# Performance work log

Hardware: AMD Instinct MI355X
Metric: run time of the kernel (lower is better)

The kernel has to match this reference:

```python
import jax, jax.numpy as jnp
import numpy as np

K = 8
EPS = 1e-5

def knn_idx(x, k):
    # x: (B, C, N) -> idx (B, N, k) nearest neighbors (incl. self)
    xt = jnp.swapaxes(x, 1, 2)  # (B, N, C)
    inner = -2.0 * jnp.einsum('bnc,bmc->bnm', xt, xt)
    xx = jnp.sum(xt * xt, axis=-1)  # (B, N)
    neg_dist = -xx[:, :, None] - inner - xx[:, None, :]
    return jax.lax.top_k(neg_dist, k)[1]

def graph_feature(x, k):
    # x: (B, C, N) -> (B, 2C, N, k)
    B, C, N = x.shape
    idx = knn_idx(x, k)  # (B, N, k)
    xt = jnp.swapaxes(x, 1, 2)  # (B, N, C)
    nb = xt[jnp.arange(B)[:, None, None], idx]  # (B, N, k, C)
    center = xt[:, :, None, :]
    feat = jnp.concatenate([nb - center, jnp.broadcast_to(center, nb.shape)], axis=-1)
    return jnp.transpose(feat, (0, 3, 1, 2))

def bn2d(h, g, b):
    m = jnp.mean(h, axis=(0, 2, 3), keepdims=True)
    v = jnp.var(h, axis=(0, 2, 3), keepdims=True)
    return g[None, :, None, None] * (h - m) * jax.lax.rsqrt(v + EPS) + b[None, :, None, None]

def bn1d(h, g, b):
    m = jnp.mean(h, axis=(0, 2), keepdims=True)
    v = jnp.var(h, axis=(0, 2), keepdims=True)
    return g[None, :, None] * (h - m) * jax.lax.rsqrt(v + EPS) + b[None, :, None]

def fps_idx(xyz, m):
    # xyz: (B, N, 3) furthest point sampling starting at index 0 -> (B, m) int32
    B, N, _ = xyz.shape
    def body(carry, _):
        dist, last = carry
        lastp = jnp.take_along_axis(xyz, last[:, None, None], axis=1)  # (B,1,3)
        d = jnp.sum((xyz - lastp) ** 2, axis=-1)
        dist = jnp.minimum(dist, d)
        nxt = jnp.argmax(dist, axis=-1).astype(jnp.int32)
        return (dist, nxt), last
    init = (jnp.full((B, N), 1e10, dtype=xyz.dtype), jnp.zeros((B,), jnp.int32))
    _, idxs = jax.lax.scan(body, init, None, length=m)
    return jnp.swapaxes(idxs, 0, 1)  # (B, m)

def fps_downsample(coor, x, m):
    # coor: (B,3,N), x: (B,C,N)
    idx = fps_idx(jnp.swapaxes(coor, 1, 2), m)  # (B, m)
    B = coor.shape[0]
    comb = jnp.concatenate([coor, x], axis=1)  # (B, 3+C, N)
    g = jnp.take_along_axis(comb, idx[:, None, :], axis=2)
    return g[:, :3], g[:, 3:]

def edge_block(h, w, g, b):
    f = graph_feature(h, K)                      # (B, 2C, N, k)
    f = jnp.einsum('oc,bcnk->bonk', w, f)        # 1x1 conv2d, no bias
    f = jax.nn.leaky_relu(bn2d(f, g, b), 0.2)
    return jnp.max(f, axis=-1)                   # (B, O, N)

def setup_inputs() -> dict:
    key = jax.random.key(0)
    ks = jax.random.split(key, 16)
    H = 2048
    c16, c8, c4, c2 = H // 16, H // 8, H // 4, H // 2  # 128,256,512,1024
    O2 = 4096 // 2  # 2048
    def w(k, o, c):
        return jax.random.normal(k, (o, c), jnp.float32) * (1.0 / np.sqrt(c))
    inp = {
        'x': jax.random.normal(ks[0], (8, 3, 2048), jnp.float32),
        'w1': w(ks[1], c16, 6),
        'w2': w(ks[2], c16, c8),
        'w3': w(ks[3], c8, c8),
        'w4': w(ks[4], c4, c4),
        'w5': w(ks[5], O2, c2),
        'rw1': w(ks[6], c16, c16),
        'rw2': w(ks[7], c8, c16),
        'rw3': w(ks[8], c4, c8),
    }
    for i, (nm, ch) in enumerate([('1', c16), ('2', c16), ('3', c8), ('4', c4), ('5', O2)]):
        kk = jax.random.split(ks[9 + i], 2)
        inp['g' + nm] = 1.0 + 0.1 * jax.random.normal(kk[0], (ch,), jnp.float32)
        inp['b' + nm] = 0.1 * jax.random.normal(kk[1], (ch,), jnp.float32)
    return inp

def reference(x, w1, w2, w3, w4, w5, rw1, rw2, rw3, g1, b1, g2, b2, g3, b3, g4, b4, g5, b5):
    coor = x
    x1 = edge_block(x, w1, g1, b1)
    x2 = edge_block(x1, w2, g2, b2) + jnp.einsum('oc,bcn->bon', rw1, x1)
    x3 = edge_block(x2, w3, g3, b3) + jnp.einsum('oc,bcn->bon', rw2, x2)
    x4 = edge_block(x3, w4, g4, b4) + jnp.einsum('oc,bcn->bon', rw3, x3)
    h = jnp.concatenate([x1, x2, x3, x4], axis=1)  # (B, 1024, N)
    h = jax.nn.leaky_relu(bn1d(jnp.einsum('oc,bcn->bon', w5, h), g5, b5), 0.2)
    for m in (512, 256, 128):
        coor, h = fps_downsample(coor, h, m)
    f = jnp.concatenate([jnp.max(h, axis=-1), jnp.mean(h, axis=-1)], axis=1)  # (B, 4096)
    return coor, f
```

## Files before the change

### kernel.cpp

```cpp
#include <hip/hip_runtime.h>
#include <float.h>

#define NPTS 2048
#define NB 8
#define KNN 8

__device__ __forceinline__ float leakyf(float x){ return x > 0.f ? x : 0.2f*x; }

#define BET(v1,i1,v2,i2) (((v1)>(v2)) || ((v1)==(v2) && (i1)<(i2)))

__device__ __forceinline__ void ins8(float tv[8], int tix[8], float v, int ci)
{
    if (BET(v,ci,tv[7],tix[7])){
        tv[7]=v; tix[7]=ci;
#pragma unroll
        for (int q=7;q>=1;q--){
            if (BET(tv[q],tix[q],tv[q-1],tix[q-1])){
                float t=tv[q]; tv[q]=tv[q-1]; tv[q-1]=t;
                int ti=tix[q]; tix[q]=tix[q-1]; tix[q-1]=ti;
            }
        }
    }
}

__device__ __forceinline__ void merge_write8(float tv[8], int tix[8], int lane,
                                             int* __restrict__ dst)
{
#pragma unroll
    for (int r=0;r<8;r++){
        float bv = tv[0]; int bi = tix[0];
#pragma unroll
        for (int off=32; off; off>>=1){
            float ov = __shfl_xor(bv, off); int oi = __shfl_xor(bi, off);
            if (BET(ov,oi,bv,bi)){ bv=ov; bi=oi; }
        }
        if (tv[0]==bv && tix[0]==bi){
#pragma unroll
            for (int q=0;q<7;q++){ tv[q]=tv[q+1]; tix[q]=tix[q+1]; }
            tv[7]=-FLT_MAX; tix[7]=0x7fffffff;
        }
        if (lane==0) dst[r] = bi;
    }
}

__global__ void transpose_x(const float* __restrict__ x, float* __restrict__ xt)
{
    int g = blockIdx.x*256 + threadIdx.x;
    if (g >= NB*NPTS) return;
    int b = g >> 11, n = g & 2047;
    const float* xb = x + (long)b*3*NPTS;
    xt[g*3+0] = xb[n];
    xt[g*3+1] = xb[NPTS+n];
    xt[g*3+2] = xb[2*NPTS+n];
}

__device__ __forceinline__ unsigned long long u64max(unsigned long long a,
                                                     unsigned long long b)
{ return a > b ? a : b; }

template<int CTRL>
__device__ __forceinline__ unsigned long long dpp_max_step(unsigned long long v)
{
    unsigned plo = (unsigned)__builtin_amdgcn_update_dpp(0, (int)(unsigned)v,      CTRL, 0xF, 0xF, true);
    unsigned phi = (unsigned)__builtin_amdgcn_update_dpp(0, (int)(unsigned)(v>>32), CTRL, 0xF, 0xF, true);
    unsigned long long p = ((unsigned long long)phi << 32) | plo;
    return u64max(v, p);
}

__device__ __forceinline__ unsigned long long wave_reduce_max(unsigned long long v)
{
    v = dpp_max_step<0x111>(v);
    v = dpp_max_step<0x112>(v);
    v = dpp_max_step<0x114>(v);
    v = dpp_max_step<0x118>(v);
    v = dpp_max_step<0x142>(v);
    v = dpp_max_step<0x143>(v);
    return v;
}

template<int NPP>
__device__ void fps_stage_mw(const float4* __restrict__ pts, int m, int* sel,
                             int tid, unsigned long long* wv )
{
    float cx[NPP], cy[NPP], cz[NPP], dist[NPP];
#pragma unroll
    for (int r=0;r<NPP;r++){
        float4 p = pts[r*256 + tid];
        cx[r]=p.x; cy[r]=p.y; cz[r]=p.z; dist[r]=1e10f;
    }
    int w = tid>>6, lane = tid&63;
    int last = 0;
    if (tid==0) sel[0]=0;
    for (int i=1;i<m;i++){
        float4 lp = pts[last];
#pragma unroll
        for (int r=0;r<NPP;r++){
            float dx=__fsub_rn(cx[r],lp.x), dy=__fsub_rn(cy[r],lp.y), dz=__fsub_rn(cz[r],lp.z);
            float d = __fadd_rn(__fadd_rn(__fmul_rn(dx,dx), __fmul_rn(dy,dy)), __fmul_rn(dz,dz));
            dist[r] = fminf(dist[r], d);
        }
        unsigned long long t[(NPP+1)/2];
        if (NPP == 1){
            t[0] = ((unsigned long long)__float_as_uint(dist[0])<<32) | (unsigned)(2047 - tid);
        } else {
#pragma unroll
            for (int k=0;k<NPP/2;k++){
                unsigned long long a = ((unsigned long long)__float_as_uint(dist[2*k  ])<<32) | (unsigned)(2047 - ((2*k  )*256+tid));
                unsigned long long b = ((unsigned long long)__float_as_uint(dist[2*k+1])<<32) | (unsigned)(2047 - ((2*k+1)*256+tid));
                t[k] = u64max(a, b);
            }
#pragma unroll
            for (int s=NPP/4; s>=1; s>>=1)
#pragma unroll
                for (int k=0;k<s;k++) t[k] = u64max(t[k], t[k+s]);
        }
        unsigned long long best = wave_reduce_max(t[0]);
        if (lane==63) wv[(i&1)*4 + w] = best;
        __syncthreads();
        unsigned long long b0 = wv[(i&1)*4+0], b1 = wv[(i&1)*4+1];
        unsigned long long b2 = wv[(i&1)*4+2], b3 = wv[(i&1)*4+3];
        best = u64max(u64max(b0,b1), u64max(b2,b3));
        int win = 2047 - (int)(unsigned)best;
        last = win;
        if (tid==0) sel[i] = win;
    }
}

__global__ __launch_bounds__(256)
void knn_c3(const float* __restrict__ x, int* __restrict__ idx)
{
    __shared__ float sx[NPTS], sy[NPTS], sz[NPTS];
    int b = blockIdx.x >> 5, rblk = blockIdx.x & 31;
    const float* xb = x + (long)b*3*NPTS;
    int tid = threadIdx.x;
    for (int i=tid;i<NPTS;i+=256){
        sx[i]=xb[i]; sy[i]=xb[NPTS+i]; sz[i]=xb[2*NPTS+i];
    }
    __syncthreads();
    int w = tid>>6, lane = tid&63;
    for (int rr=0; rr<16; rr++){
        int n = rblk*64 + w*16 + rr;
        float px=sx[n], py=sy[n], pz=sz[n];
        float tv[8]; int tix[8];
#pragma unroll
        for (int i=0;i<8;i++){ tv[i]=-FLT_MAX; tix[i]=0x7fffffff; }
        for (int it=0; it<8; it++){
            int c = it*256 + lane*4;
            float4 qx = *(const float4*)&sx[c];
            float4 qy = *(const float4*)&sy[c];
            float4 qz = *(const float4*)&sz[c];
            float dx, dy, dz;
            dx=qx.x-px; dy=qy.x-py; dz=qz.x-pz;
            ins8(tv,tix, -fmaf(dx,dx,fmaf(dy,dy,dz*dz)), c+0);
            dx=qx.y-px; dy=qy.y-py; dz=qz.y-pz;
            ins8(tv,tix, -fmaf(dx,dx,fmaf(dy,dy,dz*dz)), c+1);
            dx=qx.z-px; dy=qy.z-py; dz=qz.z-pz;
            ins8(tv,tix, -fmaf(dx,dx,fmaf(dy,dy,dz*dz)), c+2);
            dx=qx.w-px; dy=qy.w-py; dz=qz.w-pz;
            ins8(tv,tix, -fmaf(dx,dx,fmaf(dy,dy,dz*dz)), c+3);
        }
        merge_write8(tv, tix, lane, idx + ((long)(b*NPTS+n))*KNN);
    }
}

__global__ void prep_w(const float* __restrict__ w, const float* __restrict__ rw,
                       float* __restrict__ wcat, int O, int C, int hasR)
{
    int t = blockIdx.x*256 + threadIdx.x;
    if (t >= O*C) return;
    int o = t / C, c = t % C;
    float a = w[o*2*C + c];
    wcat[o*C + c] = a;
    wcat[(O+o)*C + c] = w[o*2*C + C + c] - a;
    if (hasR) wcat[(2*O+o)*C + c] = rw[o*C + c];
}

__global__ void rownorm(const float* __restrict__ X, float* __restrict__ xx,
                        int lda, int C)
{
    int g = blockIdx.x*256 + threadIdx.x;
    if (g >= NB*NPTS) return;
    const float* r = X + (long)g*lda;
    float s = 0.f;
    for (int c=0;c<C;c++) s += r[c]*r[c];
    xx[g] = s;
}

template<int VEC, bool SYM>
__global__ __launch_bounds__(256)
void gemm_nt(const float* __restrict__ A, const float* __restrict__ B,
             float* __restrict__ C,
             int M, int Nc, int Kd, int lda, int ldb, int ldc,
             long sA, long sB, long sC)
{
    if (SYM && blockIdx.y > blockIdx.x) return;
    int bz = blockIdx.z;
    A += (long)bz * sA; B += (long)bz * sB; C += (long)bz * sC;
    int tm = blockIdx.y * 128, tn = blockIdx.x * 128;
    __shared__ __align__(16) float As[16][132];
    __shared__ __align__(16) float Bs[16][132];
    int tid = threadIdx.x;
    int ty = tid >> 4, tx = tid & 15;
    int cn0 = tx*4, cn1 = 64 + tx*4;
    float acc[8][8] = {};
    for (int k0 = 0; k0 < Kd; k0 += 16){
        if (VEC == 4){
#pragma unroll
            for (int i=0;i<2;i++){
                int e = tid + i*256;
                int rr = e >> 2, kq = e & 3;
                float4 av = *(const float4*)(A + (long)(tm+rr)*lda + k0 + kq*4);
                float4 bv = *(const float4*)(B + (long)(tn+rr)*ldb + k0 + kq*4);
                As[kq*4+0][rr]=av.x; As[kq*4+1][rr]=av.y; As[kq*4+2][rr]=av.z; As[kq*4+3][rr]=av.w;
                Bs[kq*4+0][rr]=bv.x; Bs[kq*4+1][rr]=bv.y; Bs[kq*4+2][rr]=bv.z; Bs[kq*4+3][rr]=bv.w;
            }
        } else {
#pragma unroll
            for (int i=0;i<8;i++){
                int e = tid + i*256;
                int kk = e & 15, rr = e >> 4;
                int ak = k0 + kk;
                As[kk][rr] = (ak < Kd) ? A[(long)(tm+rr)*lda + ak] : 0.f;
                Bs[kk][rr] = (ak < Kd) ? B[(long)(tn+rr)*ldb + ak] : 0.f;
            }
        }
        __syncthreads();
#pragma unroll
        for (int kk=0;kk<16;kk++){
            float4 a01 = *(const float4*)&As[kk][ty*8];
            float4 a23 = *(const float4*)&As[kk][ty*8+4];
            float4 b01 = *(const float4*)&Bs[kk][cn0];
            float4 b23 = *(const float4*)&Bs[kk][cn1];
            float aa[8] = {a01.x,a01.y,a01.z,a01.w,a23.x,a23.y,a23.z,a23.w};
            float bb[8] = {b01.x,b01.y,b01.z,b01.w,b23.x,b23.y,b23.z,b23.w};
#pragma unroll
            for (int i=0;i<8;i++)
#pragma unroll
                for (int j=0;j<8;j++)
                    acc[i][j] += aa[i]*bb[j];
        }
        __syncthreads();
    }
#pragma unroll
    for (int i=0;i<8;i++){
        long r = tm + ty*8 + i;
        float4 v0 = {acc[i][0],acc[i][1],acc[i][2],acc[i][3]};
        float4 v1 = {acc[i][4],acc[i][5],acc[i][6],acc[i][7]};
        *(float4*)(C + r*ldc + tn + cn0) = v0;
        *(float4*)(C + r*ldc + tn + cn1) = v1;
    }
    if (SYM && blockIdx.x != blockIdx.y){
#pragma unroll
        for (int j=0;j<4;j++){
            long r0 = tn + cn0 + j;
            long r1 = tn + cn1 + j;
            float4 u0 = {acc[0][j],  acc[1][j],  acc[2][j],  acc[3][j]};
            float4 u1 = {acc[4][j],  acc[5][j],  acc[6][j],  acc[7][j]};
            float4 u2 = {acc[0][j+4],acc[1][j+4],acc[2][j+4],acc[3][j+4]};
            float4 u3 = {acc[4][j+4],acc[5][j+4],acc[6][j+4],acc[7][j+4]};
            *(float4*)(C + r0*ldc + tm + ty*8)     = u0;
            *(float4*)(C + r0*ldc + tm + ty*8 + 4) = u1;
            *(float4*)(C + r1*ldc + tm + ty*8)     = u2;
            *(float4*)(C + r1*ldc + tm + ty*8 + 4) = u3;
        }
    }
}

__global__ __launch_bounds__(256)
void topk8(const float* __restrict__ D, const float* __restrict__ xx,
           int* __restrict__ idx, int b0)
{
    int tid = threadIdx.x, w = tid>>6, lane = tid & 63;
    int gr = blockIdx.x*4 + w;
    int b = b0 + (gr >> 11);
    const float* drow = D + (long)gr*NPTS;
    const float* xb = xx + (long)b*NPTS;
    float tv[8]; int tix[8];
#pragma unroll
    for (int i=0;i<8;i++){ tv[i]=-FLT_MAX; tix[i]=0x7fffffff; }
    for (int it=0; it<8; it++){
        int c = it*256 + lane*4;
        float4 d4 = *(const float4*)(drow + c);
        float4 x4 = *(const float4*)(xb + c);
        ins8(tv,tix, 2.f*d4.x - x4.x, c+0);
        ins8(tv,tix, 2.f*d4.y - x4.y, c+1);
        ins8(tv,tix, 2.f*d4.z - x4.z, c+2);
        ins8(tv,tix, 2.f*d4.w - x4.w, c+3);
    }
    merge_write8(tv, tix, lane, idx + ((long)(b0*NPTS) + gr)*KNN);
}

__global__ __launch_bounds__(256)
void stats_edge(const float* __restrict__ uvr, const int* __restrict__ idx,
                float* __restrict__ ps, float* __restrict__ pq,
                float* __restrict__ mxb, float* __restrict__ mnb,
                int O, int ld)
{
    int tid = threadIdx.x;
    int r0 = blockIdx.x * 128;
    float s0=0,q0=0,s1=0,q1=0;
    for (int rr=0; rr<128; rr++){
        int g = r0 + rr;
        int b = g >> 11;
        const int* ip = idx + (long)g*KNN;
        const float* vrow = uvr + (long)g*ld + O;
        const float* ub[8];
#pragma unroll
        for (int k=0;k<8;k++) ub[k] = uvr + (long)((b<<11) + ip[k])*ld;
        int o = tid;
        if (o < O){
            float vv = vrow[o];
            float mx=-FLT_MAX, mn=FLT_MAX;
#pragma unroll
            for (int k=0;k<8;k++){
                float f = ub[k][o]+vv;
                s0+=f; q0+=f*f; mx=fmaxf(mx,f); mn=fminf(mn,f);
            }
            mxb[(long)g*O+o]=mx; mnb[(long)g*O+o]=mn;
        }
        o = tid + 256;
        if (o < O){
            float vv = vrow[o];
            float mx=-FLT_MAX, mn=FLT_MAX;
#pragma unroll
            for (int k=0;k<8;k++){
                float f = ub[k][o]+vv;
                s1+=f; q1+=f*f; mx=fmaxf(mx,f); mn=fminf(mn,f);
            }
            mxb[(long)g*O+o]=mx; mnb[(long)g*O+o]=mn;
        }
    }
    if (tid < O){ ps[blockIdx.x*2048 + tid] = s0; pq[blockIdx.x*2048 + tid] = q0; }
    if (tid+256 < O){ ps[blockIdx.x*2048 + tid+256] = s1; pq[blockIdx.x*2048 + tid+256] = q1; }
}

__global__ void reduce_stats(const float* __restrict__ ps, const float* __restrict__ pq,
                             const float* __restrict__ gam, const float* __restrict__ bet,
                             float* __restrict__ ab, float* __restrict__ cb,
                             int O, int np, float invCnt)
{
    int o = blockIdx.x*256 + threadIdx.x;
    if (o >= O) return;
    float s=0.f, q=0.f;
    for (int p=0;p<np;p++){ s += ps[p*2048 + o]; q += pq[p*2048 + o]; }
    float m = s * invCnt;
    float var = q * invCnt - m*m;
    float a = gam[o] * rsqrtf(var + 1e-5f);
    ab[o] = a;
    cb[o] = bet[o] - m*a;
}

__global__ void finalize_edge(const float* __restrict__ mxb, const float* __restrict__ mnb,
                              const float* __restrict__ uvr,
                              const float* __restrict__ ab, const float* __restrict__ cb,
                              float* __restrict__ hcat, int lgO, int ld, int hoff, int hasR)
{
    long t = (long)blockIdx.x*256 + threadIdx.x;
    int O = 1 << lgO;
    int o = (int)(t & (O-1));
    int g = (int)(t >> lgO);
    float a = ab[o], c = cb[o];
    float mx = mxb[t], mn = mnb[t];
    float zz = (a > 0.f) ? (a*mx + c) : (a*mn + c);
    float outv = leakyf(zz);
    if (hasR) outv += uvr[(long)g*ld + 2*O + o];
    hcat[(long)g*1024 + hoff + o] = outv;
}

__global__ void colsum_part(const float* __restrict__ H, float* __restrict__ part)
{
    int pb = blockIdx.x;
    int tid = threadIdx.x;
    const float4* h4 = (const float4*)(H + (long)pb*128*1024);
    float4 acc = {0,0,0,0};
    for (int r=0;r<128;r++){
        float4 v = h4[r*256 + tid];
        acc.x+=v.x; acc.y+=v.y; acc.z+=v.z; acc.w+=v.w;
    }
    ((float4*)part)[pb*256 + tid] = acc;
}
__global__ void colsum_fin(const float* __restrict__ part, float* __restrict__ hbar)
{
    int tid = threadIdx.x;
    float4 acc = {0,0,0,0};
    for (int p=0;p<128;p++){
        float4 v = ((const float4*)part)[p*256 + tid];
        acc.x+=v.x; acc.y+=v.y; acc.z+=v.z; acc.w+=v.w;
    }
    ((float4*)hbar)[tid] = acc;
}

struct FpsSh {
    float4 pts1[2048]; float4 pts2[512]; float4 pts3[256];
    int sel1[512]; int sel2[256]; int sel3[128];
    unsigned long long wv[8];
};
struct GramSh { __align__(16) float As[32][132]; __align__(16) float Bs[32][132]; };
union ShU { FpsSh f; GramSh g; };

__global__ __launch_bounds__(256)
void gram_fps(const float* __restrict__ A, float* __restrict__ P,
              const float* __restrict__ x, int* __restrict__ idxF,
              float* __restrict__ coorOut)
{
    __shared__ ShU sh;
    int tid = threadIdx.x;
    if (blockIdx.x < 8){
        int b = blockIdx.x;
        const float* xb = x + (long)b*3*NPTS;
        for (int i=tid;i<2048;i+=256)
            sh.f.pts1[i] = make_float4(xb[i], xb[NPTS+i], xb[2*NPTS+i], 0.f);
        __syncthreads();
        fps_stage_mw<8>(sh.f.pts1, 512, sh.f.sel1, tid, sh.f.wv);
        __syncthreads();
        for (int i=tid;i<512;i+=256) sh.f.pts2[i] = sh.f.pts1[sh.f.sel1[i]];
        __syncthreads();
        fps_stage_mw<2>(sh.f.pts2, 256, sh.f.sel2, tid, sh.f.wv);
        __syncthreads();
        for (int i=tid;i<256;i+=256) sh.f.pts3[i] = sh.f.pts2[sh.f.sel2[i]];
        __syncthreads();
        fps_stage_mw<1>(sh.f.pts3, 128, sh.f.sel3, tid, sh.f.wv);
        __syncthreads();
        for (int i=tid;i<128;i+=256){
            int gi = sh.f.sel1[sh.f.sel2[sh.f.sel3[i]]];
            idxF[b*128+i] = gi;
            float4 p = sh.f.pts1[gi];
            coorOut[(long)b*384 + 0*128 + i] = p.x;
            coorOut[(long)b*384 + 1*128 + i] = p.y;
            coorOut[(long)b*384 + 2*128 + i] = p.z;
        }
        return;
    }
    int id8 = blockIdx.x - 8;
    int bx = id8 & 7, by = (id8 >> 3) & 7, bz = id8 >> 6;
    if (by < bx) return;
    int ti = by*128, tj = bx*128;
    int ty = tid>>4, tx = tid&15;
    float acc[8][8] = {};
    const float* Abase = A + (long)bz*1024*1024;
    for (int k0=0; k0<1024; k0+=32){
#pragma unroll
        for (int i=0;i<4;i++){
            int e = tid + i*256;
            int mm = e>>5, c4 = (e&31)*4;
            const float* arow = Abase + (long)(k0+mm)*1024;
            *(float4*)&sh.g.As[mm][c4] = *(const float4*)(arow + ti + c4);
            *(float4*)&sh.g.Bs[mm][c4] = *(const float4*)(arow + tj + c4);
        }
        __syncthreads();
#pragma unroll
        for (int mm=0;mm<32;mm++){
            float4 a01 = *(const float4*)&sh.g.As[mm][ty*8];
            float4 a23 = *(const float4*)&sh.g.As[mm][ty*8+4];
            float4 b01 = *(const float4*)&sh.g.Bs[mm][tx*4];
            float4 b23 = *(const float4*)&sh.g.Bs[mm][64+tx*4];
            float aa[8] = {a01.x,a01.y,a01.z,a01.w,a23.x,a23.y,a23.z,a23.w};
            float bb[8] = {b01.x,b01.y,b01.z,b01.w,b23.x,b23.y,b23.z,b23.w};
#pragma unroll
            for (int i=0;i<8;i++)
#pragma unroll
                for (int j=0;j<8;j++)
                    acc[i][j] += aa[i]*bb[j];
        }
        __syncthreads();
    }
    float* Pp = P + ((long)bz<<20);
#pragma unroll
    for (int i=0;i<8;i++){
        long r = ti + ty*8 + i;
        float4 v0 = {acc[i][0],acc[i][1],acc[i][2],acc[i][3]};
        float4 v1 = {acc[i][4],acc[i][5],acc[i][6],acc[i][7]};
        *(float4*)(Pp + r*1024 + tj + tx*4)      = v0;
        *(float4*)(Pp + r*1024 + tj + 64 + tx*4) = v1;
    }
}

__global__ void greduce(const float* __restrict__ P, float* __restrict__ G)
{
    long i4 = (long)blockIdx.x*256 + threadIdx.x;
    float4 a = ((const float4*)P)[i4];
    for (int p=1;p<16;p++){
        float4 v = ((const float4*)P)[((long)p<<18) + i4];
        a.x+=v.x; a.y+=v.y; a.z+=v.z; a.w+=v.w;
    }
    ((float4*)G)[i4] = a;
}

__global__ void mirror_g(float* __restrict__ G)
{
    __shared__ float t[64][65];
    int q = blockIdx.x, I = 0, acc = 15;
    while (q >= acc){ q -= acc; acc--; I++; }
    int J = I + 1 + q;
    int tid = threadIdx.x;
#pragma unroll
    for (int k=0;k<16;k++){
        int e = tid + k*256;
        int sr = e>>6, sc = e&63;
        t[sr][sc] = G[(long)(J*64+sr)*1024 + I*64+sc];
    }
    __syncthreads();
#pragma unroll
    for (int k=0;k<16;k++){
        int e = tid + k*256;
        int dr = e>>6, dc = e&63;
        G[(long)(I*64+dr)*1024 + J*64+dc] = t[dc][dr];
    }
}

__global__ void bn5_prep(const float* __restrict__ w5, const float* __restrict__ T,
                         const float* __restrict__ hbar,
                         const float* __restrict__ g5, const float* __restrict__ b5,
                         float* __restrict__ ab, float* __restrict__ cb)
{
    int w = threadIdx.x>>6, lane = threadIdx.x&63;
    int n = blockIdx.x*4 + w;
    const float4* wr = (const float4*)(w5 + (long)n*1024);
    const float4* tr = (const float4*)(T  + (long)n*1024);
    const float4* hb = (const float4*)hbar;
    float s1=0.f, s2=0.f;
    for (int i=lane;i<256;i+=64){
        float4 wv = wr[i], t4 = tr[i], hv = hb[i];
        s1 += wv.x*hv.x + wv.y*hv.y + wv.z*hv.z + wv.w*hv.w;
        s2 += wv.x*t4.x + wv.y*t4.y + wv.z*t4.z + wv.w*t4.w;
    }
#pragma unroll
    for (int off=32; off; off>>=1){
        s1 += __shfl_xor(s1, off);
        s2 += __shfl_xor(s2, off);
    }
    if (lane==0){
        float m = s1*(1.f/16384.f);
        float qq = s2*(1.f/16384.f);
        float var = qq - m*m;
        float a = g5[n]*rsqrtf(var+1e-5f);
        ab[n]=a; cb[n]=b5[n]-m*a;
    }
}

__global__ void gather_rows(const float* __restrict__ src, const int* __restrict__ idxF,
                            float* __restrict__ dst)
{
    int r = blockIdx.x;
    int b = r >> 7;
    int srow = (b<<11) + idxF[r];
    const float4* s = (const float4*)(src + (long)srow*1024);
    float4* d = (float4*)(dst + (long)r*1024);
    for (int c=threadIdx.x; c<256; c+=256) d[c] = s[c];
}

__global__ void finalize_f(const float* __restrict__ zsel, const float* __restrict__ ab,
                           const float* __restrict__ cb, float* __restrict__ out)
{
    int b = blockIdx.x >> 3, oc = blockIdx.x & 7;
    int o = oc*256 + threadIdx.x;
    float a = ab[o], c = cb[o];
    float mx = -FLT_MAX, sm = 0.f;
    const float* zp = zsel + (long)b*128*2048 + o;
    for (int i=0;i<128;i++){
        float v = leakyf(a*zp[(long)i*2048] + c);
        mx = fmaxf(mx, v); sm += v;
    }
    out[b*4096 + o] = mx;
    out[b*4096 + 2048 + o] = sm * (1.f/128.f);
}

extern "C" void kernel_launch(void* const* d_in, const int* in_sizes, int n_in,
                              void* d_out, int out_size, void* d_ws, size_t ws_size,
                              hipStream_t stream)
{
    (void)in_sizes; (void)n_in; (void)out_size; (void)ws_size;
    const float* x   = (const float*)d_in[0];
    const float* w1  = (const float*)d_in[1];
    const float* w2  = (const float*)d_in[2];
    const float* w3  = (const float*)d_in[3];
    const float* w4  = (const float*)d_in[4];
    const float* w5  = (const float*)d_in[5];
    const float* rw1 = (const float*)d_in[6];
    const float* rw2 = (const float*)d_in[7];
    const float* rw3 = (const float*)d_in[8];
    const float* g1  = (const float*)d_in[9];  const float* b1 = (const float*)d_in[10];
    const float* g2  = (const float*)d_in[11]; const float* b2 = (const float*)d_in[12];
    const float* g3  = (const float*)d_in[13]; const float* b3 = (const float*)d_in[14];
    const float* g4  = (const float*)d_in[15]; const float* b4 = (const float*)d_in[16];
    const float* g5  = (const float*)d_in[17]; const float* b5 = (const float*)d_in[18];
    float* out = (float*)d_out;

    char* wsb = (char*)d_ws;
    size_t off = 0;
    auto alloc = [&](size_t bytes)->char* {
        char* p = wsb + off;
        off += (bytes + 255) & ~(size_t)255;
        return p;
    };
    float* xt    = (float*)alloc((size_t)16384*3*4);
    float* hcat  = (float*)alloc((size_t)16384*1024*4);
    float* uvr   = (float*)alloc((size_t)16384*1536*4);
    float* Dbuf  = uvr;
    float* gramP = uvr;
    float* G     = (float*)alloc((size_t)1024*1024*4);
    float* T     = (float*)alloc((size_t)2048*1024*4);
    float* zselA = (float*)alloc((size_t)1024*1024*4);
    float* zsel  = (float*)alloc((size_t)1024*2048*4);
    float* mxb   = (float*)alloc((size_t)16384*512*4);
    float* mnb   = (float*)alloc((size_t)16384*512*4);
    float* xx    = (float*)alloc((size_t)16384*4);
    int*   idx   = (int*)  alloc((size_t)16384*8*4);
    float* wcat  = (float*)alloc((size_t)1536*256*4);
    float* ps    = (float*)alloc((size_t)128*2048*4);
    float* pq    = (float*)alloc((size_t)128*2048*4);
    float* cspart= (float*)alloc((size_t)128*1024*4);
    float* hbar  = (float*)alloc((size_t)1024*4);
    float* ab    = (float*)alloc((size_t)2048*4);
    float* cb    = (float*)alloc((size_t)2048*4);
    int*   idxF  = (int*)  alloc((size_t)1024*4);

    transpose_x<<<64, 256, 0, stream>>>(x, xt);

    struct EB {
        const float* X; int lda, C, O, lgO, hoff, hasR;
        const float* w; const float* rw; const float* g; const float* bb;
    };
    EB eb[4] = {
        { xt,        3,    3,   128, 7, 0,   0, w1, nullptr, g1, b1 },
        { hcat+0,    1024, 128, 128, 7, 128, 1, w2, rw1,     g2, b2 },
        { hcat+128,  1024, 128, 256, 8, 256, 1, w3, rw2,     g3, b3 },
        { hcat+256,  1024, 256, 512, 9, 512, 1, w4, rw3,     g4, b4 },
    };
    for (int i=0;i<4;i++){
        EB e = eb[i];
        int ld = (2 + e.hasR) * e.O;
        int tot = e.O * e.C;
        prep_w<<<(tot+255)/256, 256, 0, stream>>>(e.w, e.rw, wcat, e.O, e.C, e.hasR);
        if (i == 0){
            knn_c3<<<256, 256, 0, stream>>>(x, idx);
            gemm_nt<1,false><<<dim3(ld/128, 128, 1), 256, 0, stream>>>(
                e.X, wcat, uvr, 16384, ld, e.C, e.lda, e.C, ld, 0, 0, 0);
        } else {
            rownorm<<<64, 256, 0, stream>>>(e.X, xx, e.lda, e.C);
            for (int b0=0; b0<8; b0+=2){
                const float* Ab = e.X + (long)b0*NPTS*e.lda;
                gemm_nt<4,true><<<dim3(16,16,2), 256, 0, stream>>>(
                    Ab, Ab, Dbuf, 2048, 2048, e.C, e.lda, e.lda, 2048,
                    (long)NPTS*e.lda, (long)NPTS*e.lda, (long)NPTS*NPTS);
                topk8<<<1024, 256, 0, stream>>>(Dbuf, xx, idx, b0);
            }
            gemm_nt<4,false><<<dim3(ld/128, 128, 1), 256, 0, stream>>>(
                e.X, wcat, uvr, 16384, ld, e.C, e.lda, e.C, ld, 0, 0, 0);
        }
        stats_edge<<<128, 256, 0, stream>>>(uvr, idx, ps, pq, mxb, mnb, e.O, ld);
        reduce_stats<<<(e.O+255)/256, 256, 0, stream>>>(ps, pq, e.g, e.bb, ab, cb,
                                                        e.O, 128, 1.f/131072.f);
        finalize_edge<<<64*e.O, 256, 0, stream>>>(mxb, mnb, uvr, ab, cb, hcat,
                                                  e.lgO, ld, e.hoff, e.hasR);
    }

    colsum_part<<<128, 256, 0, stream>>>(hcat, cspart);
    colsum_fin<<<1, 256, 0, stream>>>(cspart, hbar);
    gram_fps<<<8 + 8*8*16, 256, 0, stream>>>(hcat, gramP, x, idxF, out);
    greduce<<<1024, 256, 0, stream>>>(gramP, G);
    mirror_g<<<120, 256, 0, stream>>>(G);
    gemm_nt<4,false><<<dim3(8,16,1), 256, 0, stream>>>(
        w5, G, T, 2048, 1024, 1024, 1024, 1024, 1024, 0, 0, 0);
    bn5_prep<<<512, 256, 0, stream>>>(w5, T, hbar, g5, b5, ab, cb);
    gather_rows<<<1024, 256, 0, stream>>>(hcat, idxF, zselA);
    gemm_nt<4,false><<<dim3(16,8,1), 256, 0, stream>>>(
        zselA, w5, zsel, 1024, 2048, 1024, 1024, 1024, 2048, 0, 0, 0);
    finalize_f<<<64, 256, 0, stream>>>(zsel, ab, cb, out + 3072);
}
```

Before: 3.524 ms.

## Use bf16 MFMA for Gram matrix and move FPS into the last edge GEMM launch

The Gram matrix of the concatenated features is now computed with bf16 MFMA instructions over swizzled LDS tiles, one upper-triangle tile per batch, and the column-sum work is fused into the same launch. FPS runs alongside the layer-4 uvr GEMM blocks instead of alongside the Gram blocks, so it overlaps with different work. kNN for the first layer uses four times as many smaller blocks, and the distance GEMM and top-k batches are processed four at a time instead of two. Rounding the Gram inputs to bf16 lowers the precision of the BN5 statistics, which may move results outside tolerance.

```diff
diff --git a/kernel.cpp b/kernel.cpp
--- a/kernel.cpp
+++ b/kernel.cpp
@@ -5,7 +5,15 @@
 #define NB 8
 #define KNN 8
 
+typedef short bf16x8 __attribute__((ext_vector_type(8)));
+typedef float f32x4  __attribute__((ext_vector_type(4)));
+
 __device__ __forceinline__ float leakyf(float x){ return x > 0.f ? x : 0.2f*x; }
+
+__device__ __forceinline__ unsigned short f2bf(float f){
+    unsigned u = __float_as_uint(f);
+    return (unsigned short)((u + 0x7FFF + ((u>>16)&1)) >> 16);
+}
 
 #define BET(v1,i1,v2,i2) (((v1)>(v2)) || ((v1)==(v2) && (i1)<(i2)))
 
@@ -80,7 +88,7 @@
 
 template<int NPP>
 __device__ void fps_stage_mw(const float4* __restrict__ pts, int m, int* sel,
-                             int tid, unsigned long long* wv )
+                             int tid, unsigned long long* wv)
 {
     float cx[NPP], cy[NPP], cz[NPP], dist[NPP];
 #pragma unroll
@@ -126,11 +134,46 @@
     }
 }
 
+struct FpsSh {
+    float4 pts1[2048]; float4 pts2[512]; float4 pts3[256];
+    int sel1[512]; int sel2[256]; int sel3[128];
+    unsigned long long wv[8];
+};
+struct GemmSh { __align__(16) float As[16][132]; __align__(16) float Bs[16][132]; };
+union ShU { FpsSh f; GemmSh g; };
+
+__device__ void fps_block(const float* __restrict__ x, int* __restrict__ idxF,
+                          float* __restrict__ coorOut, int b, int tid, FpsSh& sh)
+{
+    const float* xb = x + (long)b*3*NPTS;
+    for (int i=tid;i<2048;i+=256)
+        sh.pts1[i] = make_float4(xb[i], xb[NPTS+i], xb[2*NPTS+i], 0.f);
+    __syncthreads();
+    fps_stage_mw<8>(sh.pts1, 512, sh.sel1, tid, sh.wv);
+    __syncthreads();
+    for (int i=tid;i<512;i+=256) sh.pts2[i] = sh.pts1[sh.sel1[i]];
+    __syncthreads();
+    fps_stage_mw<2>(sh.pts2, 256, sh.sel2, tid, sh.wv);
+    __syncthreads();
+    for (int i=tid;i<256;i+=256) sh.pts3[i] = sh.pts2[sh.sel2[i]];
+    __syncthreads();
+    fps_stage_mw<1>(sh.pts3, 128, sh.sel3, tid, sh.wv);
+    __syncthreads();
+    for (int i=tid;i<128;i+=256){
+        int gi = sh.sel1[sh.sel2[sh.sel3[i]]];
+        idxF[b*128+i] = gi;
+        float4 p = sh.pts1[gi];
+        coorOut[(long)b*384 + 0*128 + i] = p.x;
+        coorOut[(long)b*384 + 1*128 + i] = p.y;
+        coorOut[(long)b*384 + 2*128 + i] = p.z;
+    }
+}
+
 __global__ __launch_bounds__(256)
 void knn_c3(const float* __restrict__ x, int* __restrict__ idx)
 {
     __shared__ float sx[NPTS], sy[NPTS], sz[NPTS];
-    int b = blockIdx.x >> 5, rblk = blockIdx.x & 31;
+    int b = blockIdx.x >> 7, rblk = blockIdx.x & 127;
     const float* xb = x + (long)b*3*NPTS;
     int tid = threadIdx.x;
     for (int i=tid;i<NPTS;i+=256){
@@ -138,8 +181,8 @@
     }
     __syncthreads();
     int w = tid>>6, lane = tid&63;
-    for (int rr=0; rr<16; rr++){
-        int n = rblk*64 + w*16 + rr;
+    for (int rr=0; rr<4; rr++){
+        int n = rblk*16 + w*4 + rr;
         float px=sx[n], py=sy[n], pz=sz[n];
         float tv[8]; int tix[8];
 #pragma unroll
@@ -187,19 +230,12 @@
 }
 
 template<int VEC, bool SYM>
-__global__ __launch_bounds__(256)
-void gemm_nt(const float* __restrict__ A, const float* __restrict__ B,
-             float* __restrict__ C,
-             int M, int Nc, int Kd, int lda, int ldb, int ldc,
-             long sA, long sB, long sC)
-{
-    if (SYM && blockIdx.y > blockIdx.x) return;
-    int bz = blockIdx.z;
-    A += (long)bz * sA; B += (long)bz * sB; C += (long)bz * sC;
-    int tm = blockIdx.y * 128, tn = blockIdx.x * 128;
-    __shared__ __align__(16) float As[16][132];
-    __shared__ __align__(16) float Bs[16][132];
-    int tid = threadIdx.x;
+__device__ __forceinline__ void gemm_body(
+    float (*As)[132], float (*Bs)[132],
+    const float* __restrict__ A, const float* __restrict__ B, float* __restrict__ C,
+    int Kd, int lda, int ldb, int ldc, int bx, int by, int tid)
+{
+    int tm = by * 128, tn = bx * 128;
     int ty = tid >> 4, tx = tid & 15;
     int cn0 = tx*4, cn1 = 64 + tx*4;
     float acc[8][8] = {};
@@ -249,7 +285,7 @@
         *(float4*)(C + r*ldc + tn + cn0) = v0;
         *(float4*)(C + r*ldc + tn + cn1) = v1;
     }
-    if (SYM && blockIdx.x != blockIdx.y){
+    if (SYM && bx != by){
 #pragma unroll
         for (int j=0;j<4;j++){
             long r0 = tn + cn0 + j;
@@ -266,6 +302,37 @@
     }
 }
 
+template<int VEC, bool SYM>
+__global__ __launch_bounds__(256)
+void gemm_nt(const float* __restrict__ A, const float* __restrict__ B,
+             float* __restrict__ C,
+             int Kd, int lda, int ldb, int ldc,
+             long sA, long sB, long sC)
+{
+    if (SYM && blockIdx.y > blockIdx.x) return;
+    __shared__ GemmSh sh;
+    int bz = blockIdx.z;
+    gemm_body<VEC,SYM>(sh.As, sh.Bs, A + (long)bz*sA, B + (long)bz*sB,
+                       C + (long)bz*sC, Kd, lda, ldb, ldc,
+                       blockIdx.x, blockIdx.y, threadIdx.x);
+}
+
+__global__ __launch_bounds__(256)
+void uvr_fps(const float* __restrict__ A, const float* __restrict__ B,
+             float* __restrict__ C, int Kd, int lda, int ldb, int ldc, int nx,
+             const float* __restrict__ x, int* __restrict__ idxF,
+             float* __restrict__ coorOut)
+{
+    __shared__ ShU sh;
+    if (blockIdx.x < 8){
+        fps_block(x, idxF, coorOut, blockIdx.x, threadIdx.x, sh.f);
+        return;
+    }
+    int id = blockIdx.x - 8;
+    gemm_body<4,false>(sh.g.As, sh.g.Bs, A, B, C, Kd, lda, ldb, ldc,
+                       id % nx, id / nx, threadIdx.x);
+}
+
 __global__ __launch_bounds__(256)
 void topk8(const float* __restrict__ D, const float* __restrict__ xx,
            int* __restrict__ idx, int b0)
@@ -367,18 +434,6 @@
     hcat[(long)g*1024 + hoff + o] = outv;
 }
 
-__global__ void colsum_part(const float* __restrict__ H, float* __restrict__ part)
-{
-    int pb = blockIdx.x;
-    int tid = threadIdx.x;
-    const float4* h4 = (const float4*)(H + (long)pb*128*1024);
-    float4 acc = {0,0,0,0};
-    for (int r=0;r<128;r++){
-        float4 v = h4[r*256 + tid];
-        acc.x+=v.x; acc.y+=v.y; acc.z+=v.z; acc.w+=v.w;
-    }
-    ((float4*)part)[pb*256 + tid] = acc;
-}
 __global__ void colsum_fin(const float* __restrict__ part, float* __restrict__ hbar)
 {
     int tid = threadIdx.x;
@@ -390,88 +445,83 @@
     ((float4*)hbar)[tid] = acc;
 }
 
-struct FpsSh {
-    float4 pts1[2048]; float4 pts2[512]; float4 pts3[256];
-    int sel1[512]; int sel2[256]; int sel3[128];
-    unsigned long long wv[8];
-};
-struct GramSh { __align__(16) float As[32][132]; __align__(16) float Bs[32][132]; };
-union ShU { FpsSh f; GramSh g; };
-
 __global__ __launch_bounds__(256)
-void gram_fps(const float* __restrict__ A, float* __restrict__ P,
-              const float* __restrict__ x, int* __restrict__ idxF,
-              float* __restrict__ coorOut)
-{
-    __shared__ ShU sh;
+void gram_colsum(const float* __restrict__ H, float* __restrict__ P,
+                 float* __restrict__ cspart)
+{
+    __shared__ __align__(16) unsigned short As[128][40];
+    __shared__ __align__(16) unsigned short Bs[128][40];
     int tid = threadIdx.x;
-    if (blockIdx.x < 8){
-        int b = blockIdx.x;
-        const float* xb = x + (long)b*3*NPTS;
-        for (int i=tid;i<2048;i+=256)
-            sh.f.pts1[i] = make_float4(xb[i], xb[NPTS+i], xb[2*NPTS+i], 0.f);
+    if (blockIdx.x >= 288){
+        int pb = blockIdx.x - 288;
+        const float4* h4 = (const float4*)(H + (long)pb*128*1024);
+        float4 acc = {0,0,0,0};
+        for (int r=0;r<128;r++){
+            float4 v = h4[r*256 + tid];
+            acc.x+=v.x; acc.y+=v.y; acc.z+=v.z; acc.w+=v.w;
+        }
+        ((float4*)cspart)[pb*256 + tid] = acc;
+        return;
+    }
+    int bz = blockIdx.x / 36, t36 = blockIdx.x % 36;
+    int I = 0, q = t36, accq = 8;
+    while (q >= accq){ q -= accq; accq--; I++; }
+    int ti = (I + q)*128, tj = I*128;
+    int w = tid>>6, lane = tid&63;
+    int wr = (w>>1)*64, wc = (w&1)*64;
+    f32x4 acc[16];
+#pragma unroll
+    for (int i=0;i<16;i++) acc[i] = (f32x4){0.f,0.f,0.f,0.f};
+    const float* Hc = H + (long)bz*2048*1024;
+    for (int m0=0; m0<2048; m0+=32){
+#pragma unroll
+        for (int it=0; it<4; it++){
+            int e = tid + it*256;
+            int mm = e >> 5;
+            int c4 = (e & 31) * 4;
+            const float* row = Hc + (long)(m0+mm)*1024;
+            float4 av = *(const float4*)(row + ti + c4);
+            float4 bv = *(const float4*)(row + tj + c4);
+            int mg = mm >> 3, ml = mm & 7;
+            float fa[4] = {av.x, av.y, av.z, av.w};
+            float fb[4] = {bv.x, bv.y, bv.z, bv.w};
+#pragma unroll
+            for (int qq=0; qq<4; qq++){
+                int ia = c4 + qq;
+                int pos = ((mg ^ ((ia>>2)&3))<<3) + ml;
+                As[ia][pos] = f2bf(fa[qq]);
+                Bs[ia][pos] = f2bf(fb[qq]);
+            }
+        }
         __syncthreads();
-        fps_stage_mw<8>(sh.f.pts1, 512, sh.f.sel1, tid, sh.f.wv);
+        bf16x8 af[4], bf[4];
+#pragma unroll
+        for (int f=0; f<4; f++){
+            int ra = wr + f*16 + (lane&15);
+            int ga = ((lane>>4) ^ ((ra>>2)&3)) << 3;
+            af[f] = *(const bf16x8*)&As[ra][ga];
+            int rb = wc + f*16 + (lane&15);
+            int gb = ((lane>>4) ^ ((rb>>2)&3)) << 3;
+            bf[f] = *(const bf16x8*)&Bs[rb][gb];
+        }
+#pragma unroll
+        for (int fi=0; fi<4; fi++)
+#pragma unroll
+        for (int fj=0; fj<4; fj++)
+            acc[fi*4+fj] = __builtin_amdgcn_mfma_f32_16x16x32_bf16(
+                af[fi], bf[fj], acc[fi*4+fj], 0, 0, 0);
         __syncthreads();
-        for (int i=tid;i<512;i+=256) sh.f.pts2[i] = sh.f.pts1[sh.f.sel1[i]];
-        __syncthreads();
-        fps_stage_mw<2>(sh.f.pts2, 256, sh.f.sel2, tid, sh.f.wv);
-        __syncthreads();
-        for (int i=tid;i<256;i+=256) sh.f.pts3[i] = sh.f.pts2[sh.f.sel2[i]];
-        __syncthreads();
-        fps_stage_mw<1>(sh.f.pts3, 128, sh.f.sel3, tid, sh.f.wv);
-        __syncthreads();
-        for (int i=tid;i<128;i+=256){
-            int gi = sh.f.sel1[sh.f.sel2[sh.f.sel3[i]]];
-            idxF[b*128+i] = gi;
-            float4 p = sh.f.pts1[gi];
-            coorOut[(long)b*384 + 0*128 + i] = p.x;
-            coorOut[(long)b*384 + 1*128 + i] = p.y;
-            coorOut[(long)b*384 + 2*128 + i] = p.z;
-        }
-        return;
-    }
-    int id8 = blockIdx.x - 8;
-    int bx = id8 & 7, by = (id8 >> 3) & 7, bz = id8 >> 6;
-    if (by < bx) return;
-    int ti = by*128, tj = bx*128;
-    int ty = tid>>4, tx = tid&15;
-    float acc[8][8] = {};
-    const float* Abase = A + (long)bz*1024*1024;
-    for (int k0=0; k0<1024; k0+=32){
-#pragma unroll
-        for (int i=0;i<4;i++){
-            int e = tid + i*256;
-            int mm = e>>5, c4 = (e&31)*4;
-            const float* arow = Abase + (long)(k0+mm)*1024;
-            *(float4*)&sh.g.As[mm][c4] = *(const float4*)(arow + ti + c4);
-            *(float4*)&sh.g.Bs[mm][c4] = *(const float4*)(arow + tj + c4);
-        }
-        __syncthreads();
-#pragma unroll
-        for (int mm=0;mm<32;mm++){
-            float4 a01 = *(const float4*)&sh.g.As[mm][ty*8];
-            float4 a23 = *(const float4*)&sh.g.As[mm][ty*8+4];
-            float4 b01 = *(const float4*)&sh.g.Bs[mm][tx*4];
-            float4 b23 = *(const float4*)&sh.g.Bs[mm][64+tx*4];
-            float aa[8] = {a01.x,a01.y,a01.z,a01.w,a23.x,a23.y,a23.z,a23.w};
-            float bb[8] = {b01.x,b01.y,b01.z,b01.w,b23.x,b23.y,b23.z,b23.w};
-#pragma unroll
-            for (int i=0;i<8;i++)
-#pragma unroll
-                for (int j=0;j<8;j++)
-                    acc[i][j] += aa[i]*bb[j];
-        }
-        __syncthreads();
     }
     float* Pp = P + ((long)bz<<20);
 #pragma unroll
-    for (int i=0;i<8;i++){
-        long r = ti + ty*8 + i;
-        float4 v0 = {acc[i][0],acc[i][1],acc[i][2],acc[i][3]};
-        float4 v1 = {acc[i][4],acc[i][5],acc[i][6],acc[i][7]};
-        *(float4*)(Pp + r*1024 + tj + tx*4)      = v0;
-        *(float4*)(Pp + r*1024 + tj + 64 + tx*4) = v1;
+    for (int fi=0; fi<4; fi++)
+#pragma unroll
+    for (int fj=0; fj<4; fj++){
+        int row0 = ti + wr + fi*16 + (lane>>4)*4;
+        int col  = tj + wc + fj*16 + (lane&15);
+#pragma unroll
+        for (int r4=0; r4<4; r4++)
+            Pp[(long)(row0+r4)*1024 + col] = acc[fi*4+fj][r4];
     }
 }
 
@@ -479,7 +529,7 @@
 {
     long i4 = (long)blockIdx.x*256 + threadIdx.x;
     float4 a = ((const float4*)P)[i4];
-    for (int p=1;p<16;p++){
+    for (int p=1;p<8;p++){
         float4 v = ((const float4*)P)[((long)p<<18) + i4];
         a.x+=v.x; a.y+=v.y; a.z+=v.z; a.w+=v.w;
     }
@@ -630,23 +680,28 @@
     for (int i=0;i<4;i++){
         EB e = eb[i];
         int ld = (2 + e.hasR) * e.O;
+        int nx = ld / 128;
         int tot = e.O * e.C;
         prep_w<<<(tot+255)/256, 256, 0, stream>>>(e.w, e.rw, wcat, e.O, e.C, e.hasR);
         if (i == 0){
-            knn_c3<<<256, 256, 0, stream>>>(x, idx);
-            gemm_nt<1,false><<<dim3(ld/128, 128, 1), 256, 0, stream>>>(
-                e.X, wcat, uvr, 16384, ld, e.C, e.lda, e.C, ld, 0, 0, 0);
+            knn_c3<<<1024, 256, 0, stream>>>(x, idx);
+            gemm_nt<1,false><<<dim3(nx, 128, 1), 256, 0, stream>>>(
+                e.X, wcat, uvr, e.C, e.lda, e.C, ld, 0, 0, 0);
         } else {
             rownorm<<<64, 256, 0, stream>>>(e.X, xx, e.lda, e.C);
-            for (int b0=0; b0<8; b0+=2){
+            for (int b0=0; b0<8; b0+=4){
                 const float* Ab = e.X + (long)b0*NPTS*e.lda;
-                gemm_nt<4,true><<<dim3(16,16,2), 256, 0, stream>>>(
-                    Ab, Ab, Dbuf, 2048, 2048, e.C, e.lda, e.lda, 2048,
+                gemm_nt<4,true><<<dim3(16,16,4), 256, 0, stream>>>(
+                    Ab, Ab, Dbuf, e.C, e.lda, e.lda, 2048,
                     (long)NPTS*e.lda, (long)NPTS*e.lda, (long)NPTS*NPTS);
-                topk8<<<1024, 256, 0, stream>>>(Dbuf, xx, idx, b0);
+                topk8<<<2048, 256, 0, stream>>>(Dbuf, xx, idx, b0);
             }
-            gemm_nt<4,false><<<dim3(ld/128, 128, 1), 256, 0, stream>>>(
-                e.X, wcat, uvr, 16384, ld, e.C, e.lda, e.C, ld, 0, 0, 0);
+            if (i == 3)
+                uvr_fps<<<8 + nx*128, 256, 0, stream>>>(
+                    e.X, wcat, uvr, e.C, e.lda, e.C, ld, nx, x, idxF, out);
+            else
+                gemm_nt<4,false><<<dim3(nx, 128, 1), 256, 0, stream>>>(
+                    e.X, wcat, uvr, e.C, e.lda, e.C, ld, 0, 0, 0);
         }
         stats_edge<<<128, 256, 0, stream>>>(uvr, idx, ps, pq, mxb, mnb, e.O, ld);
         reduce_stats<<<(e.O+255)/256, 256, 0, stream>>>(ps, pq, e.g, e.bb, ab, cb,
@@ -655,16 +710,15 @@
                                                   e.lgO, ld, e.hoff, e.hasR);
     }
 
-    colsum_part<<<128, 256, 0, stream>>>(hcat, cspart);
+    gram_colsum<<<288 + 128, 256, 0, stream>>>(hcat, gramP, cspart);
     colsum_fin<<<1, 256, 0, stream>>>(cspart, hbar);
-    gram_fps<<<8 + 8*8*16, 256, 0, stream>>>(hcat, gramP, x, idxF, out);
     greduce<<<1024, 256, 0, stream>>>(gramP, G);
     mirror_g<<<120, 256, 0, stream>>>(G);
     gemm_nt<4,false><<<dim3(8,16,1), 256, 0, stream>>>(
-        w5, G, T, 2048, 1024, 1024, 1024, 1024, 1024, 0, 0, 0);
+        w5, G, T, 1024, 1024, 1024, 1024, 0, 0, 0);
     bn5_prep<<<512, 256, 0, stream>>>(w5, T, hbar, g5, b5, ab, cb);
     gather_rows<<<1024, 256, 0, stream>>>(hcat, idxF, zselA);
     gemm_nt<4,false><<<dim3(16,8,1), 256, 0, stream>>>(
-        zselA, w5, zsel, 1024, 2048, 1024, 1024, 1024, 2048, 0, 0, 0);
+        zselA, w5, zsel, 1024, 1024, 1024, 2048, 0, 0, 0);
     finalize_f<<<64, 256, 0, stream>>>(zsel, ab, cb, out + 3072);
 }
```

Result: faster. 3.052 ms (-13.4%).
